# Performance work log

Measured on AMD Instinct MI355X. Metric: run time of the kernel, lower is better.

Reference implementation:

```python
import jax, jax.numpy as jnp
import numpy as np

N_E = 512
E_DIM = 128
LEGACY = 0.2
B, T = 64, 1024


def setup_inputs() -> dict:
    key = jax.random.key(0)
    k1, k2 = jax.random.split(key, 2)
    key_soft = jax.random.normal(k1, (B, T, E_DIM), dtype=jnp.float32)
    emb_weight = jax.random.uniform(k2, (N_E + 1, E_DIM), dtype=jnp.float32,
                                    minval=-1.0 / N_E, maxval=1.0 / N_E)
    zero_ts_mask = jnp.zeros((B,), dtype=jnp.bool_)
    return {"key_soft": key_soft, "emb_weight": emb_weight, "zero_ts_mask": zero_ts_mask}


def _neighbor_indices(d, zero_ts_mask, n_e):
    # d: [B, T, n_e+1] (no grad needed; only used for int index selection)
    ind0 = jnp.clip(jnp.argmin(d[:, 0, :], axis=1), 0, n_e - 1)
    ind0 = jnp.where(zero_ts_mask, 0, ind0)

    def step(ind, d_t):  # ind: [B], d_t: [B, n_e+1]
        d_here = jnp.take_along_axis(d_t, ind[:, None], axis=1)[:, 0]
        ind_next = jnp.clip(ind + 1, 0, n_e - 1)
        d_next = jnp.take_along_axis(d_t, ind_next[:, None], axis=1)[:, 0]
        ind_new = jnp.where(d_here <= d_next, ind, ind_next)
        return ind_new, ind_new

    _, rest = jax.lax.scan(step, ind0, jnp.swapaxes(d[:, 1:, :], 0, 1))  # [T-1, B]
    return jnp.concatenate([ind0[None, :], rest], axis=0).T  # [B, T]


def reference(key_soft, emb_weight, zero_ts_mask):
    sg = jax.lax.stop_gradient
    n_e = emb_weight.shape[0] - 1
    b, t, e_dim = key_soft.shape

    # squared-distance matrix: [B, T, n_e+1]
    d = (jnp.sum(key_soft ** 2, axis=-1, keepdims=True)
         + jnp.sum(emb_weight ** 2, axis=1)
         - 2.0 * jnp.einsum('btd,nd->btn', key_soft, emb_weight))
    d_ng = sg(d)

    min_indices = jnp.argmin(d_ng, axis=-1)                 # [B, T] (over full n_e+1)
    enc = _neighbor_indices(d_ng, zero_ts_mask, n_e)        # [B, T]

    key_hard_here = emb_weight[enc]                                  # [B, T, D]
    key_hard_next = emb_weight[jnp.clip(enc + 1, 0, n_e - 1)]        # [B, T, D]
    key_min = emb_weight[min_indices]                                # [B, T, D]

    def vq_loss(kh):
        return (jnp.sum((sg(key_soft) - kh) ** 2, axis=-1)
                + jnp.sum((key_soft - sg(kh)) ** 2, axis=-1) * LEGACY)

    loss_here_base = vq_loss(key_hard_here)
    loss_next_base = vq_loss(key_hard_next)

    energy = (jnp.sum((sg(key_soft) - key_hard_next) ** 2, axis=-1)
              - jnp.sum((sg(key_soft) - key_hard_here) ** 2, axis=-1)
              + (jnp.sum((key_soft - sg(key_hard_next)) ** 2, axis=-1)
                 - jnp.sum((key_soft - sg(key_hard_here)) ** 2, axis=-1)) * LEGACY)

    change = (enc[:, 1:] - enc[:, :-1]) != 0
    same_hard_mask = jnp.where(change, 0.0, 1.0)
    energy_change = (energy[:, 1:] - energy[:, :-1]) * same_hard_mask
    loss_energy_descent = jnp.maximum(energy_change + 1e-06 / n_e,
                                      jnp.zeros_like(energy_change)).mean()
    energy_mean = energy.mean()

    loss_min_indices = vq_loss(key_min)
    loss_min_here = jnp.where(loss_min_indices < loss_here_base, loss_min_indices, 0.0)
    loss_min_next = jnp.where(loss_min_indices < loss_next_base, loss_min_indices, 0.0)

    loss_here = loss_here_base - loss_next_base - loss_min_here
    loss_next = loss_next_base - loss_here_base - loss_min_next

    key_hard = key_soft + sg(key_hard_here - key_soft)  # straight-through

    v = jnp.max(jnp.max(enc, axis=1) - jnp.min(enc, axis=1))
    return (key_hard, enc, v, loss_here, loss_next, energy_mean, loss_energy_descent)
```

## Files before the change

### kernel.cpp

```cpp
#include <hip/hip_runtime.h>
#include <cfloat>
#include <cstdint>

#define B_  64
#define T_  1024
#define D_  128
#define NE  512
#define P_  (B_*T_)

#define O_KH   0
#define O_ENC  (P_*D_)
#define O_V    (O_ENC + P_)
#define O_LH   (O_V + 1)
#define O_LN   (O_LH + P_)
#define O_EM   (O_LN + P_)
#define O_LED  (O_EM + 1)

typedef __attribute__((ext_vector_type(8))) short bf16x8;
typedef __attribute__((ext_vector_type(4))) float floatx4;
typedef unsigned long long u64;

__device__ __forceinline__ void pack8(const float4& a, const float4& b,
                                      uint4& h, uint4& l)
{
    float v[8] = {a.x,a.y,a.z,a.w,b.x,b.y,b.z,b.w};
    unsigned hw[4], lw[4];
    #pragma unroll
    for (int e = 0; e < 4; e++) {
        const unsigned ua = __float_as_uint(v[2*e]);
        const unsigned ub = __float_as_uint(v[2*e+1]);
        const float fa = __uint_as_float(ua & 0xffff0000u);
        const float fb = __uint_as_float(ub & 0xffff0000u);
        const unsigned da = __float_as_uint(v[2*e]   - fa);
        const unsigned db = __float_as_uint(v[2*e+1] - fb);
        hw[e] = (ub & 0xffff0000u) | (ua >> 16);
        lw[e] = (db & 0xffff0000u) | (da >> 16);
    }
    h = make_uint4(hw[0],hw[1],hw[2],hw[3]);
    l = make_uint4(lw[0],lw[1],lw[2],lw[3]);
}

__device__ __forceinline__ u64 shflx64(u64 v, int d)
{
    const int lo = __shfl_xor((int)(unsigned)(v & 0xffffffffULL), d);
    const int hi = __shfl_xor((int)(unsigned)(v >> 32), d);
    return ((u64)(unsigned)hi << 32) | (unsigned)lo;
}

__device__ __forceinline__ unsigned sortkey(float f)
{
    const unsigned b = __float_as_uint(f);
    return b ^ (unsigned)(((int)b >> 31) | (int)0x80000000);
}

__global__ __launch_bounds__(64) void kFG(const float* __restrict__ emb,
                                          unsigned short* __restrict__ ehi,
                                          unsigned short* __restrict__ elo,
                                          float* __restrict__ sq,
                                          unsigned* __restrict__ cnt)
{
    if (blockIdx.x == 0 && threadIdx.x == 0) *cnt = 0u;
    const int t = blockIdx.x * 64 + threadIdx.x;
    const int n = t >> 2, kst = t & 3;
    const float4* src = (const float4*)(emb + (size_t)n * D_ + kst * 32);
    float ss = 0.f;
    #pragma unroll
    for (int g = 0; g < 4; g++) {
        const float4 a = src[2*g], b = src[2*g+1];
        ss += a.x*a.x + a.y*a.y + a.z*a.z + a.w*a.w
            + b.x*b.x + b.y*b.y + b.z*b.z + b.w*b.w;
        uint4 h, l;
        pack8(a, b, h, l);
        const int f = ((n >> 4) * 4 + kst) * 4 + g;
        *(uint4*)(ehi + (size_t)f*128 + (size_t)(n & 15)*8) = h;
        *(uint4*)(elo + (size_t)f*128 + (size_t)(n & 15)*8) = l;
    }
    ss += __shfl_xor(ss, 1);
    ss += __shfl_xor(ss, 2);
    if (kst == 0) sq[n] = ss;
}

__global__ __launch_bounds__(512, 4) void kA(const float* __restrict__ ks,
                                          const float* __restrict__ sq,
                                          const unsigned short* __restrict__ ehi,
                                          const unsigned short* __restrict__ elo,
                                          u64* __restrict__ bits,
                                          float* __restrict__ sfirst,
                                          float* __restrict__ slast,
                                          unsigned* __restrict__ mins,
                                          unsigned short* __restrict__ mini16)
{
    __shared__ unsigned short Bh[32*128];
    __shared__ unsigned short Bl[32*128];

    const int tid  = threadIdx.x;
    const int lane = tid & 63;
    const int wv   = tid >> 6;
    const int m    = lane & 15;
    const int q    = lane >> 4;
    const int bid  = blockIdx.x;
    const int h    = bid >> 10;
    const int pt   = bid & 1023;
    const int p0   = pt * 64 + h * 32;
    const int ch   = wv;
    const int nb   = ch * 64;

    {
        const int srow = tid >> 4;
        const int scg  = tid & 15;
        const float4* sp = (const float4*)(ks + ((size_t)p0 + srow)*D_ + scg*8);
        uint4 hh, ll;
        pack8(sp[0], sp[1], hh, ll);
        const int cb = (srow*256 + scg*16) ^ ((srow & 7) << 4);
        *(uint4*)((char*)Bh + cb) = hh;
        *(uint4*)((char*)Bl + cb) = ll;
    }
    __syncthreads();

    floatx4 acc[4][2];
    #pragma unroll
    for (int i = 0; i < 4; i++)
        #pragma unroll
        for (int j = 0; j < 2; j++)
            #pragma unroll
            for (int r = 0; r < 4; r++) acc[i][j][r] = 0.f;

    bf16x8 ah0[4], al0[4], ah1[4], al1[4], bh[2], bl[2];

    auto loadA = [&](int kst, bf16x8* AH, bf16x8* AL) {
        #pragma unroll
        for (int i = 0; i < 4; i++) {
            const int off = (((ch*4 + i) * 4 + kst) * 4 + q) * 128 + m*8;
            AH[i] = *(const bf16x8*)(ehi + off);
            AL[i] = *(const bf16x8*)(elo + off);
        }
    };
    auto loadB = [&](int kst) {
        #pragma unroll
        for (int j = 0; j < 2; j++) {
            const int row = j*16 + m;
            const int cb = (row*256 + kst*64 + q*16) ^ ((row & 7) << 4);
            bh[j] = *(const bf16x8*)((const char*)Bh + cb);
            bl[j] = *(const bf16x8*)((const char*)Bl + cb);
        }
    };
    auto mfma3 = [&](const bf16x8* AH, const bf16x8* AL) {
        __builtin_amdgcn_s_setprio(1);
        #pragma unroll
        for (int i = 0; i < 4; i++)
            #pragma unroll
            for (int j = 0; j < 2; j++)
                acc[i][j] = __builtin_amdgcn_mfma_f32_16x16x32_bf16(AH[i], bh[j], acc[i][j], 0, 0, 0);
        #pragma unroll
        for (int i = 0; i < 4; i++)
            #pragma unroll
            for (int j = 0; j < 2; j++)
                acc[i][j] = __builtin_amdgcn_mfma_f32_16x16x32_bf16(AH[i], bl[j], acc[i][j], 0, 0, 0);
        #pragma unroll
        for (int i = 0; i < 4; i++)
            #pragma unroll
            for (int j = 0; j < 2; j++)
                acc[i][j] = __builtin_amdgcn_mfma_f32_16x16x32_bf16(AL[i], bh[j], acc[i][j], 0, 0, 0);
        __builtin_amdgcn_s_setprio(0);
    };

    loadA(0, ah0, al0);
    loadA(1, ah1, al1); loadB(0); mfma3(ah0, al0);
    loadA(2, ah0, al0); loadB(1); mfma3(ah1, al1);
    loadA(3, ah1, al1); loadB(2); mfma3(ah0, al0);
    loadB(3);
    float sa[4][4];
    #pragma unroll
    for (int i = 0; i < 4; i++) {
        const float4 s4 = *(const float4*)(sq + nb + i*16 + q*4);
        sa[i][0]=s4.x; sa[i][1]=s4.y; sa[i][2]=s4.z; sa[i][3]=s4.w;
    }
    mfma3(ah1, al1);

    #pragma unroll
    for (int j = 0; j < 2; j++) {
        float S[4][4];
        #pragma unroll
        for (int i = 0; i < 4; i++)
            #pragma unroll
            for (int r = 0; r < 4; r++)
                S[i][r] = fmaf(-2.f, acc[i][j][r], sa[i][r]);

        float nq[4], ni[4];
        #pragma unroll
        for (int i = 0; i < 4; i++) nq[i] = __shfl_down(S[i][0], 16);
        #pragma unroll
        for (int i = 0; i < 3; i++) ni[i] = __shfl(S[i+1][0], m);
        ni[3] = 0.f;

        u64 w = 0;
        #pragma unroll
        for (int i = 0; i < 4; i++) {
            #pragma unroll
            for (int r = 0; r < 3; r++)
                w |= (u64)(S[i][r] <= S[i][r+1]) << (16*i + 4*q + r);
            if (!(i == 3 && q == 3)) {
                const float nxt = (q < 3) ? nq[i] : ni[i];
                w |= (u64)(S[i][3] <= nxt) << (16*i + 4*q + 3);
            }
        }
        if (ch == 7 && q == 3) w |= 1ULL << 63;
        w |= shflx64(w, 16);
        w |= shflx64(w, 32);

        float mv = S[0][0]; int mi_ = nb + q*4;
        #pragma unroll
        for (int i = 0; i < 4; i++)
            #pragma unroll
            for (int r = 0; r < 4; r++) {
                if (i == 0 && r == 0) continue;
                const int nid = nb + 16*i + 4*q + r;
                if (S[i][r] < mv) { mv = S[i][r]; mi_ = nid; }
            }
        #pragma unroll
        for (int d = 16; d <= 32; d <<= 1) {
            const float v2 = __shfl_xor(mv, d);
            const int   i2 = __shfl_xor(mi_, d);
            if (v2 < mv || (v2 == mv && i2 < mi_)) { mv = v2; mi_ = i2; }
        }

        const size_t pg = (size_t)(p0 + j*16 + m);
        if (q == 0) {
            bits  [pg*8 + ch] = w;
            sfirst[pg*8 + ch] = S[0][0];
            mins  [pg*8 + ch] = sortkey(mv);
            mini16[pg*8 + ch] = (unsigned short)mi_;
        }
        if (q == 3) slast[pg*8 + ch] = S[3][3];
    }
}

#define KB_DECL(S) \
    u64 W0##S,W1##S,W2##S,W3##S,W4##S,W5##S,W6##S,W7##S; \
    float F0##S,F1##S,F2##S,F3##S,F4##S,F5##S,F6##S,F7##S; \
    float L0##S,L1##S,L2##S,L3##S,L4##S,L5##S,L6##S,L7##S;

#define KB_LOAD(S, T0)                                                      \
    {                                                                       \
        const int t_ = (T0) + lane;                                         \
        if (t_ < T_) {                                                      \
            const ulonglong2* bp_ = (const ulonglong2*)(bits + (p0 + t_)*8);\
            const ulonglong2 b01_ = bp_[0], b23_ = bp_[1];                  \
            const ulonglong2 b45_ = bp_[2], b67_ = bp_[3];                  \
            W0##S=b01_.x; W1##S=b01_.y; W2##S=b23_.x; W3##S=b23_.y;         \
            W4##S=b45_.x; W5##S=b45_.y; W6##S=b67_.x; W7##S=b67_.y;         \
            const float4* fp_ = (const float4*)(sfirst + (p0 + t_)*8);      \
            const float4 f0_ = fp_[0], f1_ = fp_[1];                        \
            F0##S=f0_.x; F1##S=f0_.y; F2##S=f0_.z; F3##S=f0_.w;             \
            F4##S=f1_.x; F5##S=f1_.y; F6##S=f1_.z; F7##S=f1_.w;             \
            const float4* lp_ = (const float4*)(slast + (p0 + t_)*8);       \
            const float4 l0_ = lp_[0], l1_ = lp_[1];                        \
            L0##S=l0_.x; L1##S=l0_.y; L2##S=l0_.z; L3##S=l0_.w;             \
            L4##S=l1_.x; L5##S=l1_.y; L6##S=l1_.z; L7##S=l1_.w;             \
        } else {                                                            \
            W0##S=~0ULL; W1##S=~0ULL; W2##S=~0ULL; W3##S=~0ULL;             \
            W4##S=~0ULL; W5##S=~0ULL; W6##S=~0ULL; W7##S=~0ULL;             \
            F0##S=1.f; F1##S=1.f; F2##S=1.f; F3##S=1.f;                     \
            F4##S=1.f; F5##S=1.f; F6##S=1.f; F7##S=1.f;                     \
            L0##S=0.f; L1##S=0.f; L2##S=0.f; L3##S=0.f;                     \
            L4##S=0.f; L5##S=0.f; L6##S=0.f; L7##S=0.f;                     \
        }                                                                   \
    }

#define KB_SCAN(S, T0)                                                      \
    {                                                                       \
                \
        W0##S |= (u64)(L0##S <= F1##S) << 63;                               \
        W1##S |= (u64)(L1##S <= F2##S) << 63;                               \
        W2##S |= (u64)(L2##S <= F3##S) << 63;                               \
        W3##S |= (u64)(L3##S <= F4##S) << 63;                               \
        W4##S |= (u64)(L4##S <= F5##S) << 63;                               \
        W5##S |= (u64)(L5##S <= F6##S) << 63;                               \
        W6##S |= (u64)(L6##S <= F7##S) << 63;                               \
        const int wsel_ = cur >> 6;                                         \
        const int off0_ = cur & 63;                                         \
        u64 a_ = W0##S;                                                     \
        a_ = (wsel_ == 1) ? W1##S : a_;                                     \
        a_ = (wsel_ == 2) ? W2##S : a_;                                     \
        a_ = (wsel_ == 3) ? W3##S : a_;                                     \
        a_ = (wsel_ == 4) ? W4##S : a_;                                     \
        a_ = (wsel_ == 5) ? W5##S : a_;                                     \
        a_ = (wsel_ == 6) ? W6##S : a_;                                     \
        a_ = (wsel_ == 7) ? W7##S : a_;                                     \
        u64 bn_ = ~0ULL;                                                    \
        bn_ = (wsel_ == 0) ? W1##S : bn_;                                   \
        bn_ = (wsel_ == 1) ? W2##S : bn_;                                   \
        bn_ = (wsel_ == 2) ? W3##S : bn_;                                   \
        bn_ = (wsel_ == 3) ? W4##S : bn_;                                   \
        bn_ = (wsel_ == 4) ? W5##S : bn_;                                   \
        bn_ = (wsel_ == 5) ? W6##S : bn_;                                   \
        bn_ = (wsel_ == 6) ? W7##S : bn_;                                   \
        const u64 u_ = (off0_ == 0) ? a_                                    \
                     : ((a_ >> off0_) | (bn_ << (64 - off0_)));             \
        const unsigned ulo_ = (unsigned)u_;                                 \
        const unsigned uhi_ = (unsigned)(u_ >> 32);                         \
        int doff_ = 0;                                                      \
        int myenc_ = cur;                                                   \
        _Pragma("unroll")                                                   \
        for (int j_ = 0; j_ < 64; j_++) {                                   \
            const unsigned slo_ = (unsigned)__builtin_amdgcn_readlane((int)ulo_, j_); \
            const unsigned shi_ = (unsigned)__builtin_amdgcn_readlane((int)uhi_, j_); \
            const u64 word_ = ((u64)shi_ << 32) | slo_;                     \
            const int bit_ = (int)((word_ >> doff_) & 1ULL);                \
            doff_ += 1 - bit_;                                              \
            if (lane == j_) myenc_ = cur + doff_;                           \
        }                                                                   \
        cur += doff_;                                                       \
        const int t_ = (T0) + lane;                                         \
        if (t_ < T_) {                                                      \
            enci[p0 + t_] = myenc_;                                         \
            out[O_ENC + p0 + t_] = (float)myenc_;                           \
        }                                                                   \
    }

__global__ __launch_bounds__(64) void kB(const float* __restrict__ ks,
                                         const float* __restrict__ emb,
                                         const unsigned char* __restrict__ mask,
                                         const u64* __restrict__ bits,
                                         const float* __restrict__ sfirst,
                                         const float* __restrict__ slast,
                                         const unsigned* __restrict__ mins,
                                         const unsigned short* __restrict__ mini16,
                                         int* __restrict__ enci,
                                         float* __restrict__ out)
{
    const int b    = blockIdx.x;
    const int lane = threadIdx.x;
    const size_t p0 = (size_t)b * T_;

    KB_DECL(A)
    KB_DECL(B)

    KB_LOAD(A, 1)
    KB_LOAD(B, 65)

    const float2 e = ((const float2*)(emb + (size_t)512*D_))[lane];
    const float2 k = ((const float2*)(ks  + p0*D_))[lane];
    float s5 = e.x*(e.x - 2.f*k.x) + e.y*(e.y - 2.f*k.y);
    #pragma unroll
    for (int m = 32; m >= 1; m >>= 1) s5 += __shfl_xor(s5, m);

    u64 kk = ~0ULL;
    if (lane < 8)       kk = ((u64)mins[p0*8 + lane] << 32) | (u64)mini16[p0*8 + lane];
    else if (lane == 8) kk = ((u64)sortkey(s5) << 32) | 512ULL;
    #pragma unroll
    for (int d = 1; d <= 8; d <<= 1) {
        const u64 o = shflx64(kk, d);
        kk = (o < kk) ? o : kk;
    }
    const int mi = __shfl((int)(unsigned)(kk & 0xffffffffULL), 0);
    int cur = (mi < NE) ? mi : NE - 1;
    if (mask[b]) cur = 0;
    if (lane == 0) { enci[p0] = cur; out[O_ENC + p0] = (float)cur; }

    #pragma unroll 1
    for (int wp = 0; wp < 16; wp += 2) {
        const int t0 = 1 + wp*64;
        KB_SCAN(A, t0)
        if (wp + 2 < 16) KB_LOAD(A, t0 + 128)
        KB_SCAN(B, t0 + 64)
        if (wp + 3 < 16) KB_LOAD(B, t0 + 192)
    }
}

__global__ __launch_bounds__(256) void kC(const float* __restrict__ ks,
                                          const float* __restrict__ emb,
                                          const int* __restrict__ enci,
                                          const unsigned* __restrict__ mins,
                                          const unsigned short* __restrict__ mini16,
                                          float* __restrict__ out,
                                          float* __restrict__ energy)
{
    const int lane = threadIdx.x & 63;
    const size_t p = (size_t)blockIdx.x * 4 + (threadIdx.x >> 6);
    const int q  = lane >> 4;
    const int qm = lane & 15;

    const int eh = enci[p];
    const int en = (eh + 1 < NE) ? eh + 1 : NE - 1;
    const int row = (q == 0) ? eh : ((q == 1) ? en : 512);

    const float4* ksp = (const float4*)(ks + p*D_);
    const float4 k1 = ksp[qm*2], k2 = ksp[qm*2 + 1];
    const float4* ep = (const float4*)(emb + (size_t)row*D_);
    const float4 e1 = ep[qm*2], e2 = ep[qm*2 + 1];

    float d;
    if (q == 3) {
        d = k1.x*k1.x + k1.y*k1.y + k1.z*k1.z + k1.w*k1.w
          + k2.x*k2.x + k2.y*k2.y + k2.z*k2.z + k2.w*k2.w;
    } else {
        d = e1.x*(e1.x - 2.f*k1.x) + e1.y*(e1.y - 2.f*k1.y)
          + e1.z*(e1.z - 2.f*k1.z) + e1.w*(e1.w - 2.f*k1.w)
          + e2.x*(e2.x - 2.f*k2.x) + e2.y*(e2.y - 2.f*k2.y)
          + e2.z*(e2.z - 2.f*k2.z) + e2.w*(e2.w - 2.f*k2.w);
    }
    #pragma unroll
    for (int s = 1; s <= 8; s <<= 1) d += __shfl_xor(d, s);

    const float ph  = __shfl(d, 0);
    const float pn  = __shfl(d, 16);
    const float p5  = __shfl(d, 32);
    const float sqk = __shfl(d, 48);

    u64 kk = ~0ULL;
    if (lane < 8)       kk = ((u64)mins[p*8 + lane] << 32) | (u64)mini16[p*8 + lane];
    else if (lane == 8) kk = ((u64)sortkey(p5) << 32) | 512ULL;
    #pragma unroll
    for (int s = 1; s <= 8; s <<= 1) {
        const u64 o = shflx64(kk, s);
        kk = (o < kk) ? o : kk;
    }
    const int mi = __shfl((int)(unsigned)(kk & 0xffffffffULL), 0);

    float pm;
    if (mi == eh)      pm = ph;
    else if (mi == en) pm = pn;
    else if (mi == 512) pm = p5;
    else {
        const float4* mp = (const float4*)(emb + (size_t)mi*D_);
        const float4 m1 = mp[qm*2], m2 = mp[qm*2 + 1];
        float dm = m1.x*(m1.x - 2.f*k1.x) + m1.y*(m1.y - 2.f*k1.y)
                 + m1.z*(m1.z - 2.f*k1.z) + m1.w*(m1.w - 2.f*k1.w)
                 + m2.x*(m2.x - 2.f*k2.x) + m2.y*(m2.y - 2.f*k2.y)
                 + m2.z*(m2.z - 2.f*k2.z) + m2.w*(m2.w - 2.f*k2.w);
        #pragma unroll
        for (int s = 1; s <= 8; s <<= 1) dm += __shfl_xor(dm, s);
        pm = __shfl(dm, 0);
    }

    if (q == 0) {
        float4 o1, o2;
        o1.x = k1.x + (e1.x - k1.x); o1.y = k1.y + (e1.y - k1.y);
        o1.z = k1.z + (e1.z - k1.z); o1.w = k1.w + (e1.w - k1.w);
        o2.x = k2.x + (e2.x - k2.x); o2.y = k2.y + (e2.y - k2.y);
        o2.z = k2.z + (e2.z - k2.z); o2.w = k2.w + (e2.w - k2.w);
        ((float4*)(out + p*D_))[qm*2]     = o1;
        ((float4*)(out + p*D_))[qm*2 + 1] = o2;
    }

    if (lane == 0) {
        const float lh = 1.2f * (sqk + ph);
        const float ln = 1.2f * (sqk + pn);
        const float lm = 1.2f * (sqk + pm);
        out[O_LH + p] = lh - ln - ((pm < ph) ? lm : 0.f);
        out[O_LN + p] = ln - lh - ((pm < pn) ? lm : 0.f);
        energy[p] = 1.2f * (pn - ph);
    }
}

__global__ __launch_bounds__(256) void kD1(const float* __restrict__ energy,
                                           const int* __restrict__ enci,
                                           double2* __restrict__ part,
                                           unsigned* __restrict__ cnt,
                                           float* __restrict__ out)
{
    __shared__ double sA[256], sB[256];
    __shared__ unsigned done;
    const int p = blockIdx.x * 256 + threadIdx.x;
    const float e = energy[p];
    double se = (double)e;
    double sl = 0.0;
    if ((p & (T_-1)) < T_-1) {
        const float ec = (enci[p+1] == enci[p]) ? (energy[p+1] - e) : 0.f;
        sl = (double)fmaxf(ec + (float)(1e-6/512.0), 0.f);
    }
    sA[threadIdx.x] = se; sB[threadIdx.x] = sl;
    __syncthreads();
    for (int s = 128; s >= 1; s >>= 1) {
        if (threadIdx.x < (unsigned)s) {
            sA[threadIdx.x] += sA[threadIdx.x+s];
            sB[threadIdx.x] += sB[threadIdx.x+s];
        }
        __syncthreads();
    }
    if (threadIdx.x == 0) {
        part[blockIdx.x] = make_double2(sA[0], sB[0]);
        __threadfence();
        done = atomicAdd(cnt, 1u);
    }
    __syncthreads();
    if (done != 255u) return;

    __threadfence();
    double pvx, pvy;
    pvx = ((volatile double*)part)[2*threadIdx.x];
    pvy = ((volatile double*)part)[2*threadIdx.x + 1];
    __syncthreads();
    sA[threadIdx.x] = pvx; sB[threadIdx.x] = pvy;
    __syncthreads();
    for (int s = 128; s >= 1; s >>= 1) {
        if (threadIdx.x < (unsigned)s) {
            sA[threadIdx.x] += sA[threadIdx.x+s];
            sB[threadIdx.x] += sB[threadIdx.x+s];
        }
        __syncthreads();
    }
    if (threadIdx.x < 64) {
        int v = enci[(size_t)threadIdx.x*T_ + T_-1] - enci[(size_t)threadIdx.x*T_];
        #pragma unroll
        for (int m = 32; m >= 1; m >>= 1) {
            const int v2 = __shfl_xor(v, m);
            v = (v2 > v) ? v2 : v;
        }
        if (threadIdx.x == 0) {
            out[O_V]   = (float)v;
            out[O_EM]  = (float)(sA[0] / (double)P_);
            out[O_LED] = (float)(sB[0] / (double)(B_*(T_-1)));
        }
    }
}

extern "C" void kernel_launch(void* const* d_in, const int* in_sizes, int n_in,
                              void* d_out, int out_size, void* d_ws, size_t ws_size,
                              hipStream_t stream)
{
    const float* ks  = (const float*)d_in[0];
    const float* emb = (const float*)d_in[1];
    const unsigned char* mask = (const unsigned char*)d_in[2];

    float* out = (float*)d_out;
    char* w = (char*)d_ws;
    u64*      bits   = (u64*)     (w);
    float*    sfirst = (float*)   (w + (size_t) 4*1024*1024);
    float*    slast  = (float*)   (w + (size_t) 6*1024*1024);
    unsigned* mins   = (unsigned*)(w + (size_t) 8*1024*1024);
    unsigned short* mini16 = (unsigned short*)(w + (size_t)10*1024*1024);
    int*      enci   = (int*)     (w + (size_t)11*1024*1024);
    float*    energy = (float*)   (w + (size_t)11*1024*1024 + 256*1024);
    float*    sq     = (float*)   (w + (size_t)11*1024*1024 + 512*1024);
    double2*  part   = (double2*) (w + (size_t)11*1024*1024 + 516*1024);
    unsigned* cnt    = (unsigned*)(w + (size_t)11*1024*1024 + 520*1024);
    unsigned short* ehi = (unsigned short*)(w + (size_t)11*1024*1024 + 640*1024);
    unsigned short* elo = (unsigned short*)(w + (size_t)11*1024*1024 + 768*1024);

    kFG<<<32,   64,  0, stream>>>(emb, ehi, elo, sq, cnt);
    kA <<<2048, 512, 0, stream>>>(ks, sq, ehi, elo, bits, sfirst, slast, mins, mini16);
    kB <<<B_,   64,  0, stream>>>(ks, emb, mask, bits, sfirst, slast, mins, mini16, enci, out);
    kC <<<P_/4, 256, 0, stream>>>(ks, emb, enci, mins, mini16, out, energy);
    kD1<<<256,  256, 0, stream>>>(energy, enci, part, cnt, out);
}
```

Measured before the change: 181.0 us.

## Compute cross-chunk boundary bit in kA via LDS; deepen kB prefetch

kA now shares each wave's first distance value through shared memory and computes the cross-chunk comparison bit (bit 63) directly. This removes the sfirst/slast workspace writes in kA and their reads in the serial kB scan. kB's register prefetch goes from two 64-step stages to four, so more loads are in flight during the latency-bound sequential walk. The cost is an extra __syncthreads and a little LDS in kA, plus more live registers in kB.

```diff
diff --git a/kernel.cpp b/kernel.cpp
--- a/kernel.cpp
+++ b/kernel.cpp
@@ -85,13 +85,12 @@
                                           const unsigned short* __restrict__ ehi,
                                           const unsigned short* __restrict__ elo,
                                           u64* __restrict__ bits,
-                                          float* __restrict__ sfirst,
-                                          float* __restrict__ slast,
                                           unsigned* __restrict__ mins,
                                           unsigned short* __restrict__ mini16)
 {
     __shared__ unsigned short Bh[32*128];
     __shared__ unsigned short Bl[32*128];
+    __shared__ float S00x[8][2][16];
 
     const int tid  = threadIdx.x;
     const int lane = tid & 63;
@@ -177,6 +176,13 @@
     }
     mfma3(ah1, al1);
 
+    if (q == 0) {
+        S00x[wv][0][m] = fmaf(-2.f, acc[0][0][0], sa[0][0]);
+        S00x[wv][1][m] = fmaf(-2.f, acc[0][1][0], sa[0][0]);
+    }
+    __syncthreads();
+    const int wnx = (wv < 7) ? wv + 1 : 7;
+
     #pragma unroll
     for (int j = 0; j < 2; j++) {
         float S[4][4];
@@ -204,7 +210,11 @@
                 w |= (u64)(S[i][3] <= nxt) << (16*i + 4*q + 3);
             }
         }
-        if (ch == 7 && q == 3) w |= 1ULL << 63;
+        if (q == 3) {
+            const u64 b63 = (ch == 7) ? 1ULL
+                          : (u64)(S[3][3] <= S00x[wnx][j][m]);
+            w |= b63 << 63;
+        }
         w |= shflx64(w, 16);
         w |= shflx64(w, 32);
 
@@ -227,18 +237,14 @@
         const size_t pg = (size_t)(p0 + j*16 + m);
         if (q == 0) {
             bits  [pg*8 + ch] = w;
-            sfirst[pg*8 + ch] = S[0][0];
             mins  [pg*8 + ch] = sortkey(mv);
             mini16[pg*8 + ch] = (unsigned short)mi_;
         }
-        if (q == 3) slast[pg*8 + ch] = S[3][3];
     }
 }
 
 #define KB_DECL(S) \
-    u64 W0##S,W1##S,W2##S,W3##S,W4##S,W5##S,W6##S,W7##S; \
-    float F0##S,F1##S,F2##S,F3##S,F4##S,F5##S,F6##S,F7##S; \
-    float L0##S,L1##S,L2##S,L3##S,L4##S,L5##S,L6##S,L7##S;
+    u64 W0##S,W1##S,W2##S,W3##S,W4##S,W5##S,W6##S,W7##S;
 
 #define KB_LOAD(S, T0)                                                      \
     {                                                                       \
@@ -249,34 +255,14 @@
             const ulonglong2 b45_ = bp_[2], b67_ = bp_[3];                  \
             W0##S=b01_.x; W1##S=b01_.y; W2##S=b23_.x; W3##S=b23_.y;         \
             W4##S=b45_.x; W5##S=b45_.y; W6##S=b67_.x; W7##S=b67_.y;         \
-            const float4* fp_ = (const float4*)(sfirst + (p0 + t_)*8);      \
-            const float4 f0_ = fp_[0], f1_ = fp_[1];                        \
-            F0##S=f0_.x; F1##S=f0_.y; F2##S=f0_.z; F3##S=f0_.w;             \
-            F4##S=f1_.x; F5##S=f1_.y; F6##S=f1_.z; F7##S=f1_.w;             \
-            const float4* lp_ = (const float4*)(slast + (p0 + t_)*8);       \
-            const float4 l0_ = lp_[0], l1_ = lp_[1];                        \
-            L0##S=l0_.x; L1##S=l0_.y; L2##S=l0_.z; L3##S=l0_.w;             \
-            L4##S=l1_.x; L5##S=l1_.y; L6##S=l1_.z; L7##S=l1_.w;             \
         } else {                                                            \
             W0##S=~0ULL; W1##S=~0ULL; W2##S=~0ULL; W3##S=~0ULL;             \
             W4##S=~0ULL; W5##S=~0ULL; W6##S=~0ULL; W7##S=~0ULL;             \
-            F0##S=1.f; F1##S=1.f; F2##S=1.f; F3##S=1.f;                     \
-            F4##S=1.f; F5##S=1.f; F6##S=1.f; F7##S=1.f;                     \
-            L0##S=0.f; L1##S=0.f; L2##S=0.f; L3##S=0.f;                     \
-            L4##S=0.f; L5##S=0.f; L6##S=0.f; L7##S=0.f;                     \
         }                                                                   \
     }
 
 #define KB_SCAN(S, T0)                                                      \
     {                                                                       \
-                \
-        W0##S |= (u64)(L0##S <= F1##S) << 63;                               \
-        W1##S |= (u64)(L1##S <= F2##S) << 63;                               \
-        W2##S |= (u64)(L2##S <= F3##S) << 63;                               \
-        W3##S |= (u64)(L3##S <= F4##S) << 63;                               \
-        W4##S |= (u64)(L4##S <= F5##S) << 63;                               \
-        W5##S |= (u64)(L5##S <= F6##S) << 63;                               \
-        W6##S |= (u64)(L6##S <= F7##S) << 63;                               \
         const int wsel_ = cur >> 6;                                         \
         const int off0_ = cur & 63;                                         \
         u64 a_ = W0##S;                                                     \
@@ -322,8 +308,6 @@
                                          const float* __restrict__ emb,
                                          const unsigned char* __restrict__ mask,
                                          const u64* __restrict__ bits,
-                                         const float* __restrict__ sfirst,
-                                         const float* __restrict__ slast,
                                          const unsigned* __restrict__ mins,
                                          const unsigned short* __restrict__ mini16,
                                          int* __restrict__ enci,
@@ -335,9 +319,13 @@
 
     KB_DECL(A)
     KB_DECL(B)
+    KB_DECL(C)
+    KB_DECL(D)
 
     KB_LOAD(A, 1)
     KB_LOAD(B, 65)
+    KB_LOAD(C, 129)
+    KB_LOAD(D, 193)
 
     const float2 e = ((const float2*)(emb + (size_t)512*D_))[lane];
     const float2 k = ((const float2*)(ks  + p0*D_))[lane];
@@ -359,12 +347,16 @@
     if (lane == 0) { enci[p0] = cur; out[O_ENC + p0] = (float)cur; }
 
     #pragma unroll 1
-    for (int wp = 0; wp < 16; wp += 2) {
+    for (int wp = 0; wp < 16; wp += 4) {
         const int t0 = 1 + wp*64;
         KB_SCAN(A, t0)
-        if (wp + 2 < 16) KB_LOAD(A, t0 + 128)
+        if (wp + 4 < 16) KB_LOAD(A, t0 + 256)
         KB_SCAN(B, t0 + 64)
-        if (wp + 3 < 16) KB_LOAD(B, t0 + 192)
+        if (wp + 5 < 16) KB_LOAD(B, t0 + 320)
+        KB_SCAN(C, t0 + 128)
+        if (wp + 6 < 16) KB_LOAD(C, t0 + 384)
+        KB_SCAN(D, t0 + 192)
+        if (wp + 7 < 16) KB_LOAD(D, t0 + 448)
     }
 }
 
@@ -527,8 +519,6 @@
     float* out = (float*)d_out;
     char* w = (char*)d_ws;
     u64*      bits   = (u64*)     (w);
-    float*    sfirst = (float*)   (w + (size_t) 4*1024*1024);
-    float*    slast  = (float*)   (w + (size_t) 6*1024*1024);
     unsigned* mins   = (unsigned*)(w + (size_t) 8*1024*1024);
     unsigned short* mini16 = (unsigned short*)(w + (size_t)10*1024*1024);
     int*      enci   = (int*)     (w + (size_t)11*1024*1024);
@@ -540,8 +530,8 @@
     unsigned short* elo = (unsigned short*)(w + (size_t)11*1024*1024 + 768*1024);
 
     kFG<<<32,   64,  0, stream>>>(emb, ehi, elo, sq, cnt);
-    kA <<<2048, 512, 0, stream>>>(ks, sq, ehi, elo, bits, sfirst, slast, mins, mini16);
-    kB <<<B_,   64,  0, stream>>>(ks, emb, mask, bits, sfirst, slast, mins, mini16, enci, out);
+    kA <<<2048, 512, 0, stream>>>(ks, sq, ehi, elo, bits, mins, mini16);
+    kB <<<B_,   64,  0, stream>>>(ks, emb, mask, bits, mins, mini16, enci, out);
     kC <<<P_/4, 256, 0, stream>>>(ks, emb, enci, mins, mini16, out, energy);
     kD1<<<256,  256, 0, stream>>>(energy, enci, part, cnt, out);
 }
```

New measurement: 178.5 us. Within noise of the previous version (-1.4%).
